# Performance work log

Hardware: AMD Instinct MI355X
Metric: run time of the kernel (lower is better)

Reference implementation:

```python
import jax, jax.numpy as jnp
import numpy as np

N_HEAD = 16


def setup_inputs() -> dict:
    key = jax.random.key(0)
    k1, k2, k3 = jax.random.split(key, 3)
    B, T, C = 2, 2048, 1024
    x = jax.random.normal(k1, (B, T, C), dtype=jnp.float32)
    w_attn = jax.random.normal(k2, (C, 3 * C), dtype=jnp.float32) * 0.02
    w_proj = jax.random.normal(k3, (C, C), dtype=jnp.float32) * 0.02
    return {"x": x, "w_attn": w_attn, "w_proj": w_proj}


def reference(x, w_attn, w_proj):
    B, T, C = x.shape
    H = N_HEAD
    D = C // H
    qkv = x @ w_attn  # [B, T, 3C]
    q, k, v = jnp.split(qkv, 3, axis=2)
    q = q.reshape(B, T, H, D)
    k = k.reshape(B, T, H, D)
    v = v.reshape(B, T, H, D)
    scale = 1.0 / jnp.sqrt(jnp.asarray(D, dtype=x.dtype))
    # Full T x T score matrix, matching the 'standard_attention' path.
    att = jnp.einsum('bthd,bshd->bhts', q, k) * scale  # [B, H, T, T]
    causal = jnp.tril(jnp.ones((T, T), dtype=bool))
    att = jnp.where(causal[None, None, :, :], att, jnp.asarray(-jnp.inf, dtype=att.dtype))
    att = jax.nn.softmax(att, axis=-1)
    # dropout_p is False (== 0.0) in the original module, so no dropout applied.
    y = jnp.einsum('bhts,bshd->bthd', att, v)  # [B, T, H, D]
    y = y.reshape(B, T, C)
    return y @ w_proj
```

## Files before the change

### kernel.cpp

```cpp
#include <hip/hip_runtime.h>
#include <hip/hip_bf16.h>
#include <math.h>

#define BB 2
#define TT 2048
#define HH 16
#define DD 64
#define CC 1024
#define C3 3072

typedef __attribute__((ext_vector_type(8))) short bf16x8;
typedef __attribute__((ext_vector_type(4))) short bf16x4;
typedef __attribute__((ext_vector_type(4))) float f32x4;
typedef __attribute__((ext_vector_type(2))) unsigned int u32x2;

__device__ __forceinline__ unsigned short f2bf(float f) {
  union { float f; unsigned u; } v; v.f = f;
  unsigned r = v.u + 0x7fffu + ((v.u >> 16) & 1u);
  return (unsigned short)(r >> 16);
}
__device__ __forceinline__ unsigned pack2bf(float a, float b) {
  __hip_bfloat162 h = __float22bfloat162_rn(make_float2(a, b));
  union { __hip_bfloat162 h; unsigned u; } cv; cv.h = h;
  return cv.u;
}

__device__ __forceinline__ void async_cp16(const void* g, void* l) {
  __builtin_amdgcn_global_load_lds(
      (const __attribute__((address_space(1))) void*)g,
      (__attribute__((address_space(3))) void*)l, 16, 0, 0);
}

__global__ __launch_bounds__(256)
void prep(const float* __restrict__ x, const float* __restrict__ w_attn,
          const float* __restrict__ w_proj, unsigned short* __restrict__ xb,
          unsigned short* __restrict__ wat, unsigned short* __restrict__ wpt) {
  __shared__ __align__(16) float Ts[64][68];
  const int bx = blockIdx.x, tid = threadIdx.x;
  if (bx < 1024) {
    int i = bx * 256 + tid;
#pragma unroll
    for (int it = 0; it < 4; ++it, i += 262144) {
      const float4 v = ((const float4*)x)[i];
      bf16x4 o = {(short)f2bf(v.x), (short)f2bf(v.y),
                  (short)f2bf(v.z), (short)f2bf(v.w)};
      ((bf16x4*)xb)[i] = o;
    }
    return;
  }
  const float* W;
  unsigned short* WT;
  int Nd, bound, n0, k0;
  float s;
  if (bx < 1792) {
    const int bid = bx - 1024;
    W = w_attn; WT = wat; Nd = 3072; bound = 1024; s = 0.18033688f;
    n0 = (bid % 48) * 64; k0 = (bid / 48) * 64;
  } else {
    const int bid = bx - 1792;
    W = w_proj; WT = wpt; Nd = 1024; bound = 0; s = 1.0f;
    n0 = (bid % 16) * 64; k0 = (bid / 16) * 64;
  }
  const int rl = tid >> 4, c4 = tid & 15;
#pragma unroll
  for (int it = 0; it < 4; ++it) {
    const int r = it * 16 + rl;
    *(float4*)&Ts[r][c4 * 4] =
        *(const float4*)(W + (size_t)(k0 + r) * Nd + n0 + c4 * 4);
  }
  __syncthreads();
#pragma unroll
  for (int it = 0; it < 4; ++it) {
    const int n = it * 16 + rl;
    const float sc = (n0 + n < bound) ? s : 1.0f;
    bf16x4 o = {(short)f2bf(Ts[c4 * 4 + 0][n] * sc),
                (short)f2bf(Ts[c4 * 4 + 1][n] * sc),
                (short)f2bf(Ts[c4 * 4 + 2][n] * sc),
                (short)f2bf(Ts[c4 * 4 + 3][n] * sc)};
    *(bf16x4*)(WT + (size_t)(n0 + n) * CC + k0 + c4 * 4) = o;
  }
}

__global__ __launch_bounds__(256, 3)
void gemm_qkv(const unsigned short* __restrict__ A,
              const unsigned short* __restrict__ BT,
              unsigned short* __restrict__ Cb,
              unsigned short* __restrict__ Vout) {
  __shared__ __align__(16) unsigned short As[2 * 128 * 32];
  __shared__ __align__(16) unsigned short Bs[2 * 128 * 32];

  const int tid = threadIdx.x;
  const int w = tid >> 6, lane = tid & 63;
  const int l15 = lane & 15, quad = lane >> 4;
  const int wm = w >> 1, wn = w & 1;
  const int row0 = blockIdx.y * 128, col0 = blockIdx.x * 128;

  const int ca0 = tid, ca1 = tid + 256;
  const int ra0 = ca0 >> 2, ka0 = ((ca0 & 3) ^ ((ca0 >> 3) & 3)) * 8;
  const int ra1 = ca1 >> 2, ka1 = ((ca1 & 3) ^ ((ca1 >> 3) & 3)) * 8;
  const unsigned short* gA0 = A + (size_t)(row0 + ra0) * CC + ka0;
  const unsigned short* gA1 = A + (size_t)(row0 + ra1) * CC + ka1;
  const unsigned short* gB0 = BT + (size_t)(col0 + ra0) * CC + ka0;
  const unsigned short* gB1 = BT + (size_t)(col0 + ra1) * CC + ka1;
  const int la0 = tid * 16, la1 = tid * 16 + 4096;

  const int fro = l15 * 64 + 16 * (quad ^ ((l15 >> 1) & 3));

  f32x4 acc[4][4];
#pragma unroll
  for (int i = 0; i < 4; ++i)
#pragma unroll
    for (int j = 0; j < 4; ++j) acc[i][j] = (f32x4){0.f, 0.f, 0.f, 0.f};

  async_cp16(gA0, (char*)As + la0);
  async_cp16(gA1, (char*)As + la1);
  async_cp16(gB0, (char*)Bs + la0);
  async_cp16(gB1, (char*)Bs + la1);

  for (int i = 0; i < 32; ++i) {
    const int cur = i & 1;
    __syncthreads();

    if (i + 1 < 32) {
      const int k1 = (i + 1) * 32;
      const int ab = (cur ^ 1) * 8192;
      async_cp16(gA0 + k1, (char*)As + ab + la0);
      async_cp16(gA1 + k1, (char*)As + ab + la1);
      async_cp16(gB0 + k1, (char*)Bs + ab + la0);
      async_cp16(gB1 + k1, (char*)Bs + ab + la1);
    }

    const char* fA = (const char*)As + cur * 8192 + wm * 4096 + fro;
    const char* fB = (const char*)Bs + cur * 8192 + wn * 4096 + fro;

    bf16x8 af[4], bf[4];
#pragma unroll
    for (int mt = 0; mt < 4; ++mt) af[mt] = *(const bf16x8*)(fA + mt * 1024);
#pragma unroll
    for (int nt = 0; nt < 4; ++nt) bf[nt] = *(const bf16x8*)(fB + nt * 1024);
#pragma unroll
    for (int mt = 0; mt < 4; ++mt)
#pragma unroll
      for (int nt = 0; nt < 4; ++nt)
        acc[mt][nt] = __builtin_amdgcn_mfma_f32_16x16x32_bf16(
            af[mt], bf[nt], acc[mt][nt], 0, 0, 0);
  }

  if (col0 >= 2048) {
#pragma unroll
    for (int mt = 0; mt < 4; ++mt) {
      const int rbase = row0 + wm * 64 + mt * 16 + quad * 4;
      const int bq = rbase >> 11, t0 = rbase & 2047;
#pragma unroll
      for (int nt = 0; nt < 4; ++nt) {
        const int d = col0 + wn * 64 + nt * 16 + l15 - 2048;
        bf16x4 o = {(short)f2bf(acc[mt][nt][0]), (short)f2bf(acc[mt][nt][1]),
                    (short)f2bf(acc[mt][nt][2]), (short)f2bf(acc[mt][nt][3])};
        *(bf16x4*)(Vout + (((size_t)(bq << 10) + d) << 11) + t0) = o;
      }
    }
  } else {
#pragma unroll
    for (int mt = 0; mt < 4; ++mt) {
      const int rbase = row0 + wm * 64 + mt * 16 + quad * 4;
#pragma unroll
      for (int r = 0; r < 4; ++r) {
        unsigned short* cr =
            Cb + (size_t)(rbase + r) * C3 + col0 + wn * 64 + l15;
#pragma unroll
        for (int nt = 0; nt < 4; ++nt) cr[nt * 16] = f2bf(acc[mt][nt][r]);
      }
    }
  }
}

__global__ __launch_bounds__(256, 2)
void gemm_out(const unsigned short* __restrict__ A,
              const unsigned short* __restrict__ BT,
              float* __restrict__ Cf) {
  __shared__ __align__(16) unsigned short As[2 * 64 * 64];
  __shared__ __align__(16) unsigned short Bs[2 * 128 * 64];

  const int tid = threadIdx.x;
  const int w = tid >> 6, lane = tid & 63;
  const int l15 = lane & 15, quad = lane >> 4;
  const int wm = w >> 1, wn = w & 1;
  const int row0 = blockIdx.y * 64, col0 = blockIdx.x * 128;

  const int ca0 = tid, ca1 = tid + 256;
  const int ra0 = ca0 >> 3, ka0 = ((ca0 & 7) ^ ((ca0 >> 3) & 7)) * 8;
  const int ra1 = ca1 >> 3, ka1 = ((ca1 & 7) ^ ((ca1 >> 3) & 7)) * 8;
  const unsigned short* gA0 = A + (size_t)(row0 + ra0) * CC + ka0;
  const unsigned short* gA1 = A + (size_t)(row0 + ra1) * CC + ka1;
  const unsigned short* gB[4];
  int lb[4];
#pragma unroll
  for (int t = 0; t < 4; ++t) {
    const int c = tid + t * 256;
    const int rb = c >> 3, kb = ((c & 7) ^ ((c >> 3) & 7)) * 8;
    gB[t] = BT + (size_t)(col0 + rb) * CC + kb;
    lb[t] = c * 16;
  }
  const int la0 = tid * 16, la1 = tid * 16 + 4096;

  const int fro = l15 * 128 + ((quad ^ (l15 & 7)) << 4);

  f32x4 acc[2][4];
#pragma unroll
  for (int i = 0; i < 2; ++i)
#pragma unroll
    for (int j = 0; j < 4; ++j) acc[i][j] = (f32x4){0.f, 0.f, 0.f, 0.f};

  async_cp16(gA0, (char*)As + la0);
  async_cp16(gA1, (char*)As + la1);
#pragma unroll
  for (int t = 0; t < 4; ++t) async_cp16(gB[t], (char*)Bs + lb[t]);

  for (int i = 0; i < 16; ++i) {
    const int cur = i & 1;
    __syncthreads();

    if (i + 1 < 16) {
      const int k1 = (i + 1) * 64;
      const int ab = (cur ^ 1) * 8192, bb = (cur ^ 1) * 16384;
      async_cp16(gA0 + k1, (char*)As + ab + la0);
      async_cp16(gA1 + k1, (char*)As + ab + la1);
#pragma unroll
      for (int t = 0; t < 4; ++t) async_cp16(gB[t] + k1, (char*)Bs + bb + lb[t]);
    }

    const char* fA = (const char*)As + cur * 8192 + wm * 4096 + fro;
    const char* fB = (const char*)Bs + cur * 16384 + wn * 8192 + fro;

#pragma unroll
    for (int kh = 0; kh < 2; ++kh) {
      const int xo = kh * 64;
      bf16x8 af[2], bf[4];
#pragma unroll
      for (int mt = 0; mt < 2; ++mt)
        af[mt] = *(const bf16x8*)(fA + mt * 2048 + ((fro + xo) & 127) - (fro & 127));
#pragma unroll
      for (int nt = 0; nt < 4; ++nt)
        bf[nt] = *(const bf16x8*)(fB + nt * 2048 + ((fro + xo) & 127) - (fro & 127));
#pragma unroll
      for (int mt = 0; mt < 2; ++mt)
#pragma unroll
        for (int nt = 0; nt < 4; ++nt)
          acc[mt][nt] = __builtin_amdgcn_mfma_f32_16x16x32_bf16(
              af[mt], bf[nt], acc[mt][nt], 0, 0, 0);
    }
  }

#pragma unroll
  for (int mt = 0; mt < 2; ++mt) {
    const int rbase = row0 + wm * 32 + mt * 16 + quad * 4;
#pragma unroll
    for (int r = 0; r < 4; ++r) {
      float* cr = Cf + (size_t)(rbase + r) * CC + col0 + wn * 64 + l15;
#pragma unroll
      for (int nt = 0; nt < 4; ++nt) cr[nt * 16] = acc[mt][nt][r];
    }
  }
}

__global__ __launch_bounds__(512, 4)
void attn_mfma(const unsigned short* __restrict__ qkvb,
               const unsigned short* __restrict__ vt,
               unsigned short* __restrict__ y) {
  const int n = blockIdx.x;
  const int bh = (n & 7) + 8 * ((n >> 3) & 3);
  const int m = n >> 5;
  const int qb = (m < 8) ? m : 23 - m;
  const int b = bh >> 4, h = bh & 15;
  const int tid = threadIdx.x;
  const int w = tid >> 6;
  const int lane = tid & 63;
  const int l15 = lane & 15, quad = lane >> 4;
  const int wq = w >> 1, kh2 = w & 1;

  __shared__ __align__(16) char Kb[2 * 8192];
  __shared__ __align__(16) char Vb[2 * 8192];
  __shared__ __align__(16) char PsArena[8 * 4608];
  __shared__ float Red2[4][2][16];

  char* psw = PsArena + w * 4608;
  const int psrow = l15 * 144;

  const int lr = lane >> 3;
  const int lc = lane & 7;
  const int srcoff = ((lc ^ lr) << 4);
  const char* ksrc = (const char*)qkvb + ((size_t)(b * TT) * C3 + 1024 + h * 64) * 2;
  const char* vsrc = (const char*)vt + ((size_t)(b * HH + h) * DD * TT) * 2;

  const int fro = l15 * 128 + ((quad ^ (l15 & 7)) << 4);
  const int vxor = kh2 << 6;

  bf16x8 onesf;
#pragma unroll
  for (int jj = 0; jj < 8; ++jj) onesf[jj] = (short)0x3F80;

  const int nt = 2 * qb + 2;
  const int rmin = qb * 128 + wq * 32;
  const int rmax = rmin + 31;

  const unsigned short* qrow =
      qkvb + (size_t)(b * TT + rmin + l15) * C3 + h * DD;
  bf16x8 qf[2][2];
#pragma unroll
  for (int qg = 0; qg < 2; ++qg)
#pragma unroll
    for (int kh = 0; kh < 2; ++kh)
      qf[qg][kh] = *(const bf16x8*)(qrow + qg * 16 * C3 + kh * 32 + quad * 8);

  f32x4 O[4][2];
  f32x4 lacc[2];
#pragma unroll
  for (int dt = 0; dt < 4; ++dt)
#pragma unroll
    for (int qg = 0; qg < 2; ++qg) O[dt][qg] = (f32x4){0.f, 0.f, 0.f, 0.f};
#pragma unroll
  for (int qg = 0; qg < 2; ++qg) lacc[qg] = (f32x4){0.f, 0.f, 0.f, 0.f};

  async_cp16(ksrc + (size_t)(w * 8 + lr) * (C3 * 2) + srcoff, Kb + w * 1024);
  async_cp16(vsrc + (size_t)(w * 8 + lr) * (TT * 2) + srcoff, Vb + w * 1024);

  for (int j = 0; j < nt; ++j) {
    const int cur = j & 1;
    __syncthreads();

    if (j + 1 < nt) {
      const int key1 = (j + 1) * 64;
      async_cp16(ksrc + (size_t)(key1 + w * 8 + lr) * (C3 * 2) + srcoff,
                 Kb + (cur ^ 1) * 8192 + w * 1024);
      async_cp16(vsrc + (size_t)(w * 8 + lr) * (TT * 2) + key1 * 2 + srcoff,
                 Vb + (cur ^ 1) * 8192 + w * 1024);
    }

    const int klo = 64 * j + kh2 * 32;
    if (klo > rmax) continue;

    const char* Kc = Kb + cur * 8192;
    const char* Vc = Vb + cur * 8192;

    f32x4 S[2][2];
#pragma unroll
    for (int kt = 0; kt < 2; ++kt) {
      const int ct = kh2 * 2 + kt;
      bf16x8 k0 = *(const bf16x8*)(Kc + ct * 2048 + fro);
      bf16x8 k1 = *(const bf16x8*)(Kc + ct * 2048 + (fro ^ 64));
#pragma unroll
      for (int qg = 0; qg < 2; ++qg) {
        f32x4 z = (f32x4){-12.f, -12.f, -12.f, -12.f};
        z = __builtin_amdgcn_mfma_f32_16x16x32_bf16(k0, qf[qg][0], z, 0, 0, 0);
        z = __builtin_amdgcn_mfma_f32_16x16x32_bf16(k1, qf[qg][1], z, 0, 0, 0);
        S[kt][qg] = z;
      }
    }

    if (klo + 31 > rmin) {
#pragma unroll
      for (int kt = 0; kt < 2; ++kt)
#pragma unroll
        for (int qg = 0; qg < 2; ++qg)
#pragma unroll
          for (int r = 0; r < 4; ++r)
            if (klo + kt * 16 + quad * 4 + r > rmin + qg * 16 + l15)
              S[kt][qg][r] = -INFINITY;
    }

#pragma unroll
    for (int kt = 0; kt < 2; ++kt)
#pragma unroll
      for (int qg = 0; qg < 2; ++qg) {
        u32x2 d;
        d[0] = pack2bf(__builtin_amdgcn_exp2f(S[kt][qg][0]),
                       __builtin_amdgcn_exp2f(S[kt][qg][1]));
        d[1] = pack2bf(__builtin_amdgcn_exp2f(S[kt][qg][2]),
                       __builtin_amdgcn_exp2f(S[kt][qg][3]));
        *(u32x2*)(psw + qg * 2304 + psrow + (((kt + l15) & 3) << 5) + quad * 8) = d;
      }

    bf16x8 pf[2];
#pragma unroll
    for (int qg = 0; qg < 2; ++qg)
      pf[qg] = *(const bf16x8*)(psw + qg * 2304 + psrow +
                                ((((quad >> 1) + l15) & 3) << 5) +
                                ((quad & 1) << 4));

#pragma unroll
    for (int qg = 0; qg < 2; ++qg)
      lacc[qg] = __builtin_amdgcn_mfma_f32_16x16x32_bf16(onesf, pf[qg], lacc[qg], 0, 0, 0);
#pragma unroll
    for (int dt = 0; dt < 4; ++dt) {
      bf16x8 vf = *(const bf16x8*)(Vc + dt * 2048 + (fro ^ vxor));
#pragma unroll
      for (int qg = 0; qg < 2; ++qg)
        O[dt][qg] = __builtin_amdgcn_mfma_f32_16x16x32_bf16(vf, pf[qg], O[dt][qg], 0, 0, 0);
    }
  }

  const int epoff = l15 * 64 + ((quad ^ (l15 & 3)) << 4);
  __syncthreads();
  if (kh2) {
    char* rs = PsArena + wq * 8192;
#pragma unroll
    for (int dt = 0; dt < 4; ++dt)
#pragma unroll
      for (int qg = 0; qg < 2; ++qg)
        *(f32x4*)(rs + (dt * 2 + qg) * 1024 + epoff) = O[dt][qg];
    if (quad == 0) {
#pragma unroll
      for (int qg = 0; qg < 2; ++qg) Red2[wq][qg][l15] = lacc[qg][0];
    }
  }
  __syncthreads();
  if (!kh2) {
    const char* rs = PsArena + wq * 8192;
#pragma unroll
    for (int dt = 0; dt < 4; ++dt)
#pragma unroll
      for (int qg = 0; qg < 2; ++qg)
        O[dt][qg] += *(const f32x4*)(rs + (dt * 2 + qg) * 1024 + epoff);
    unsigned short* yr =
        y + (size_t)(b * TT + rmin + l15) * CC + h * DD + quad * 4;
#pragma unroll
    for (int qg = 0; qg < 2; ++qg) {
      const float inv = 1.0f / (lacc[qg][0] + Red2[wq][qg][l15]);
#pragma unroll
      for (int dt = 0; dt < 4; ++dt) {
        bf16x4 o = {(short)f2bf(O[dt][qg][0] * inv),
                    (short)f2bf(O[dt][qg][1] * inv),
                    (short)f2bf(O[dt][qg][2] * inv),
                    (short)f2bf(O[dt][qg][3] * inv)};
        *(bf16x4*)(yr + (size_t)qg * 16 * CC + dt * 16) = o;
      }
    }
  }
}

extern "C" void kernel_launch(void* const* d_in, const int* in_sizes, int n_in,
                              void* d_out, int out_size, void* d_ws,
                              size_t ws_size, hipStream_t stream) {
  const float* x      = (const float*)d_in[0];
  const float* w_attn = (const float*)d_in[1];
  const float* w_proj = (const float*)d_in[2];
  float* out = (float*)d_out;

  unsigned short* xb   = (unsigned short*)d_ws;
  unsigned short* wat  = xb + (size_t)4096 * 1024;
  unsigned short* wpt  = wat + (size_t)3072 * 1024;
  unsigned short* qkvb = wpt + (size_t)1024 * 1024;
  unsigned short* vt   = qkvb + (size_t)4096 * 3072;
  unsigned short* yb   = vt + (size_t)BB * HH * DD * TT;

  dim3 blk(256);

  prep<<<2048, blk, 0, stream>>>(x, w_attn, w_proj, xb, wat, wpt);

  gemm_qkv<<<dim3(C3 / 128, (BB * TT) / 128), blk, 0, stream>>>(
      xb, wat, qkvb, vt);

  attn_mfma<<<dim3(512, 1, 1), dim3(512), 0, stream>>>(qkvb, vt, yb);

  gemm_out<<<dim3(CC / 128, (BB * TT) / 64), blk, 0, stream>>>(yb, wpt, out);
}
```

Before: 174.0 us.

## Software-pipeline PV MFMA one tile behind QK and compute row sums in VALU

Restructures the attention loop so the P·V matmul for the previous key tile runs while the current tile's QK scores and exp are computed. V gets a triple-buffered shared-memory ring so the delayed PV step still reads valid data. The row-sum MFMA against a ones vector is replaced by scalar accumulation of the rounded bf16 probabilities plus a cross-quad shuffle reduction. This raises shared-memory use and adds control flow, which may reduce occupancy.

After: 174.4 us. No clear change (+0.3%).

```diff
diff --git a/kernel.cpp b/kernel.cpp
--- a/kernel.cpp
+++ b/kernel.cpp
@@ -279,7 +279,7 @@
   const int wq = w >> 1, kh2 = w & 1;
 
   __shared__ __align__(16) char Kb[2 * 8192];
-  __shared__ __align__(16) char Vb[2 * 8192];
+  __shared__ __align__(16) char Vb[3 * 8192];
   __shared__ __align__(16) char PsArena[8 * 4608];
   __shared__ float Red2[4][2][16];
 
@@ -295,13 +295,12 @@
   const int fro = l15 * 128 + ((quad ^ (l15 & 7)) << 4);
   const int vxor = kh2 << 6;
 
-  bf16x8 onesf;
-#pragma unroll
-  for (int jj = 0; jj < 8; ++jj) onesf[jj] = (short)0x3F80;
-
   const int nt = 2 * qb + 2;
   const int rmin = qb * 128 + wq * 32;
   const int rmax = rmin + 31;
+  const int jl = (rmax - kh2 * 32) >> 6;
+
+  const int pfoff = ((((quad >> 1) + l15) & 3) << 5) + ((quad & 1) << 4);
 
   const unsigned short* qrow =
       qkvb + (size_t)(b * TT + rmin + l15) * C3 + h * DD;
@@ -313,90 +312,112 @@
       qf[qg][kh] = *(const bf16x8*)(qrow + qg * 16 * C3 + kh * 32 + quad * 8);
 
   f32x4 O[4][2];
-  f32x4 lacc[2];
+  float lsum[2] = {0.f, 0.f};
 #pragma unroll
   for (int dt = 0; dt < 4; ++dt)
 #pragma unroll
     for (int qg = 0; qg < 2; ++qg) O[dt][qg] = (f32x4){0.f, 0.f, 0.f, 0.f};
-#pragma unroll
-  for (int qg = 0; qg < 2; ++qg) lacc[qg] = (f32x4){0.f, 0.f, 0.f, 0.f};
 
   async_cp16(ksrc + (size_t)(w * 8 + lr) * (C3 * 2) + srcoff, Kb + w * 1024);
   async_cp16(vsrc + (size_t)(w * 8 + lr) * (TT * 2) + srcoff, Vb + w * 1024);
 
+  int pend = -1;
   for (int j = 0; j < nt; ++j) {
-    const int cur = j & 1;
     __syncthreads();
 
     if (j + 1 < nt) {
       const int key1 = (j + 1) * 64;
       async_cp16(ksrc + (size_t)(key1 + w * 8 + lr) * (C3 * 2) + srcoff,
-                 Kb + (cur ^ 1) * 8192 + w * 1024);
+                 Kb + ((j + 1) & 1) * 8192 + w * 1024);
       async_cp16(vsrc + (size_t)(w * 8 + lr) * (TT * 2) + key1 * 2 + srcoff,
-                 Vb + (cur ^ 1) * 8192 + w * 1024);
-    }
-
-    const int klo = 64 * j + kh2 * 32;
-    if (klo > rmax) continue;
-
-    const char* Kc = Kb + cur * 8192;
-    const char* Vc = Vb + cur * 8192;
+                 Vb + ((j + 1) % 3) * 8192 + w * 1024);
+    }
+
+    const bool act = (j <= jl);
+    const bool havep = (pend >= 0);
+
+    bf16x8 pf0, pf1;
+    if (havep) {
+      pf0 = *(const bf16x8*)(psw + psrow + pfoff);
+      pf1 = *(const bf16x8*)(psw + 2304 + psrow + pfoff);
+    }
 
     f32x4 S[2][2];
-#pragma unroll
-    for (int kt = 0; kt < 2; ++kt) {
-      const int ct = kh2 * 2 + kt;
-      bf16x8 k0 = *(const bf16x8*)(Kc + ct * 2048 + fro);
-      bf16x8 k1 = *(const bf16x8*)(Kc + ct * 2048 + (fro ^ 64));
-#pragma unroll
-      for (int qg = 0; qg < 2; ++qg) {
-        f32x4 z = (f32x4){-12.f, -12.f, -12.f, -12.f};
-        z = __builtin_amdgcn_mfma_f32_16x16x32_bf16(k0, qf[qg][0], z, 0, 0, 0);
-        z = __builtin_amdgcn_mfma_f32_16x16x32_bf16(k1, qf[qg][1], z, 0, 0, 0);
-        S[kt][qg] = z;
-      }
-    }
-
-    if (klo + 31 > rmin) {
+    if (act) {
+      const char* Kc = Kb + (j & 1) * 8192;
+      const int klo = 64 * j + kh2 * 32;
+#pragma unroll
+      for (int kt = 0; kt < 2; ++kt) {
+        const int ct = kh2 * 2 + kt;
+        bf16x8 k0 = *(const bf16x8*)(Kc + ct * 2048 + fro);
+        bf16x8 k1 = *(const bf16x8*)(Kc + ct * 2048 + (fro ^ 64));
+#pragma unroll
+        for (int qg = 0; qg < 2; ++qg) {
+          f32x4 z = (f32x4){-12.f, -12.f, -12.f, -12.f};
+          z = __builtin_amdgcn_mfma_f32_16x16x32_bf16(k0, qf[qg][0], z, 0, 0, 0);
+          z = __builtin_amdgcn_mfma_f32_16x16x32_bf16(k1, qf[qg][1], z, 0, 0, 0);
+          S[kt][qg] = z;
+        }
+      }
+      if (klo + 31 > rmin) {
+#pragma unroll
+        for (int kt = 0; kt < 2; ++kt)
+#pragma unroll
+          for (int qg = 0; qg < 2; ++qg)
+#pragma unroll
+            for (int r = 0; r < 4; ++r)
+              if (klo + kt * 16 + quad * 4 + r > rmin + qg * 16 + l15)
+                S[kt][qg][r] = -INFINITY;
+      }
+    }
+
+    if (havep) {
+      const char* Vp = Vb + (pend % 3) * 8192;
+#pragma unroll
+      for (int dt = 0; dt < 4; ++dt) {
+        bf16x8 vf = *(const bf16x8*)(Vp + dt * 2048 + (fro ^ vxor));
+        O[dt][0] = __builtin_amdgcn_mfma_f32_16x16x32_bf16(vf, pf0, O[dt][0], 0, 0, 0);
+        O[dt][1] = __builtin_amdgcn_mfma_f32_16x16x32_bf16(vf, pf1, O[dt][1], 0, 0, 0);
+      }
+      pend = -1;
+    }
+
+    if (act) {
 #pragma unroll
       for (int kt = 0; kt < 2; ++kt)
 #pragma unroll
-        for (int qg = 0; qg < 2; ++qg)
-#pragma unroll
-          for (int r = 0; r < 4; ++r)
-            if (klo + kt * 16 + quad * 4 + r > rmin + qg * 16 + l15)
-              S[kt][qg][r] = -INFINITY;
-    }
-
-#pragma unroll
-    for (int kt = 0; kt < 2; ++kt)
-#pragma unroll
-      for (int qg = 0; qg < 2; ++qg) {
-        u32x2 d;
-        d[0] = pack2bf(__builtin_amdgcn_exp2f(S[kt][qg][0]),
-                       __builtin_amdgcn_exp2f(S[kt][qg][1]));
-        d[1] = pack2bf(__builtin_amdgcn_exp2f(S[kt][qg][2]),
-                       __builtin_amdgcn_exp2f(S[kt][qg][3]));
-        *(u32x2*)(psw + qg * 2304 + psrow + (((kt + l15) & 3) << 5) + quad * 8) = d;
-      }
-
-    bf16x8 pf[2];
-#pragma unroll
-    for (int qg = 0; qg < 2; ++qg)
-      pf[qg] = *(const bf16x8*)(psw + qg * 2304 + psrow +
-                                ((((quad >> 1) + l15) & 3) << 5) +
-                                ((quad & 1) << 4));
-
-#pragma unroll
-    for (int qg = 0; qg < 2; ++qg)
-      lacc[qg] = __builtin_amdgcn_mfma_f32_16x16x32_bf16(onesf, pf[qg], lacc[qg], 0, 0, 0);
+        for (int qg = 0; qg < 2; ++qg) {
+          u32x2 d;
+          d[0] = pack2bf(__builtin_amdgcn_exp2f(S[kt][qg][0]),
+                         __builtin_amdgcn_exp2f(S[kt][qg][1]));
+          d[1] = pack2bf(__builtin_amdgcn_exp2f(S[kt][qg][2]),
+                         __builtin_amdgcn_exp2f(S[kt][qg][3]));
+          lsum[qg] += __uint_as_float(d[0] << 16) +
+                      __uint_as_float(d[0] & 0xffff0000u) +
+                      __uint_as_float(d[1] << 16) +
+                      __uint_as_float(d[1] & 0xffff0000u);
+          *(u32x2*)(psw + qg * 2304 + psrow + (((kt + l15) & 3) << 5) + quad * 8) = d;
+        }
+      pend = j;
+    }
+  }
+
+  if (pend >= 0) {
+    bf16x8 pf0 = *(const bf16x8*)(psw + psrow + pfoff);
+    bf16x8 pf1 = *(const bf16x8*)(psw + 2304 + psrow + pfoff);
+    const char* Vp = Vb + (pend % 3) * 8192;
 #pragma unroll
     for (int dt = 0; dt < 4; ++dt) {
-      bf16x8 vf = *(const bf16x8*)(Vc + dt * 2048 + (fro ^ vxor));
-#pragma unroll
-      for (int qg = 0; qg < 2; ++qg)
-        O[dt][qg] = __builtin_amdgcn_mfma_f32_16x16x32_bf16(vf, pf[qg], O[dt][qg], 0, 0, 0);
-    }
+      bf16x8 vf = *(const bf16x8*)(Vp + dt * 2048 + (fro ^ vxor));
+      O[dt][0] = __builtin_amdgcn_mfma_f32_16x16x32_bf16(vf, pf0, O[dt][0], 0, 0, 0);
+      O[dt][1] = __builtin_amdgcn_mfma_f32_16x16x32_bf16(vf, pf1, O[dt][1], 0, 0, 0);
+    }
+  }
+
+#pragma unroll
+  for (int qg = 0; qg < 2; ++qg) {
+    lsum[qg] += __shfl_xor(lsum[qg], 16, 64);
+    lsum[qg] += __shfl_xor(lsum[qg], 32, 64);
   }
 
   const int epoff = l15 * 64 + ((quad ^ (l15 & 3)) << 4);
@@ -410,7 +431,7 @@
         *(f32x4*)(rs + (dt * 2 + qg) * 1024 + epoff) = O[dt][qg];
     if (quad == 0) {
 #pragma unroll
-      for (int qg = 0; qg < 2; ++qg) Red2[wq][qg][l15] = lacc[qg][0];
+      for (int qg = 0; qg < 2; ++qg) Red2[wq][qg][l15] = lsum[qg];
     }
   }
   __syncthreads();
@@ -425,7 +446,7 @@
         y + (size_t)(b * TT + rmin + l15) * CC + h * DD + quad * 4;
 #pragma unroll
     for (int qg = 0; qg < 2; ++qg) {
-      const float inv = 1.0f / (lacc[qg][0] + Red2[wq][qg][l15]);
+      const float inv = 1.0f / (lsum[qg] + Red2[wq][qg][l15]);
 #pragma unroll
       for (int dt = 0; dt < 4; ++dt) {
         bf16x4 o = {(short)f2bf(O[dt][qg][0] * inv),
```
